# Optimization experiments

Hardware: AMD Instinct MI355X
Metric: run time of the kernel (lower is better)

Reference implementation:

```python
import jax, jax.numpy as jnp
import numpy as np

NEG_SLOPE = 0.1

def _leaky(x):
    return jnp.where(x >= 0, x, NEG_SLOPE * x)

def setup_inputs() -> dict:
    key = jax.random.key(0)
    ks = jax.random.split(key, 16)
    B, N, H, W, C = 4, 128, 32, 32, 64
    inp = {
        "image": jax.random.normal(ks[0], (B, 3, H, W), dtype=jnp.float32),
        "coords": jax.random.uniform(ks[1], (B, N, 2), dtype=jnp.float32),
        "w1": jax.random.normal(ks[2], (C, 7), dtype=jnp.float32) * 0.2,
        "b1": jax.random.normal(ks[3], (C,), dtype=jnp.float32) * 0.05,
        "w2": jax.random.normal(ks[4], (C, C), dtype=jnp.float32) * 0.1,
        "b2": jax.random.normal(ks[5], (C,), dtype=jnp.float32) * 0.05,
        "w3": jax.random.normal(ks[6], (C, C), dtype=jnp.float32) * 0.1,
        "b3": jax.random.normal(ks[7], (C,), dtype=jnp.float32) * 0.05,
        "w4": jax.random.normal(ks[8], (C, C), dtype=jnp.float32) * 0.1,
        "b4": jax.random.normal(ks[9], (C,), dtype=jnp.float32) * 0.05,
        "w5": jax.random.normal(ks[10], (C, C), dtype=jnp.float32) * 0.1,
        "b5": jax.random.normal(ks[11], (C,), dtype=jnp.float32) * 0.05,
        "wl": jax.random.normal(ks[12], (3, C), dtype=jnp.float32) * 0.1,
        "bl": jax.random.normal(ks[13], (3,), dtype=jnp.float32) * 0.05,
    }
    return inp

def reference(image, coords, w1, b1, w2, b2, w3, b3, w4, b4, w5, b5, wl, bl):
    B, C_img, H, W = image.shape
    _, N, D = coords.shape
    # position encoding: channel 0 = row/(H-1), channel 1 = col/(W-1)
    row = (jnp.arange(H, dtype=jnp.float32) / (H - 1))[:, None] * jnp.ones((1, W), jnp.float32)
    col = jnp.ones((H, 1), jnp.float32) * (jnp.arange(W, dtype=jnp.float32) / (W - 1))[None, :]
    pos = jnp.stack([row, col], axis=0)  # [2,H,W]
    # x5: [B,5,H,W] = image ++ pos
    x5 = jnp.concatenate([image, jnp.broadcast_to(pos[None], (B, 2, H, W))], axis=1)
    # First 1x1 conv: split weight into image/pos part (5 ch) and coord part (2 ch);
    # avoids materializing the expanded [B*N,7,H,W] input (same math as conv on concat).
    img_part = jnp.einsum('oc,bchw->bohw', w1[:, :5], x5)          # [B,c,H,W]
    crd_part = jnp.einsum('od,bnd->bno', w1[:, 5:], coords)         # [B,N,c]
    h = _leaky(img_part[:, None] + crd_part[:, :, :, None, None] + b1[None, None, :, None, None])  # [B,N,c,H,W]
    for wi, bi in ((w2, b2), (w3, b3), (w4, b4), (w5, b5)):
        h = _leaky(jnp.einsum('oc,bnchw->bnohw', wi, h) + bi[None, None, :, None, None])
    pooled = jnp.mean(h, axis=(-2, -1))                             # [B,N,c] (AdaptiveAvgPool2d(1,1)+Flatten)
    pred = jax.nn.sigmoid(jnp.einsum('oc,bnc->bno', wl, pooled) + bl)  # [B,N,3]
    return jnp.transpose(pred, (0, 2, 1))                           # [B,3,N]
```

## Files before the change

kernel.cpp:

```cpp
#include <hip/hip_runtime.h>
#include <math.h>


typedef float  f32x4  __attribute__((ext_vector_type(4)));
typedef f32x4  f32x4a __attribute__((may_alias));
typedef __bf16 bf16x8 __attribute__((ext_vector_type(8)));
typedef bf16x8 bf16x8a __attribute__((may_alias));
typedef __bf16 bf16x4 __attribute__((ext_vector_type(4)));
typedef bf16x4 bf16x4a __attribute__((may_alias));
typedef float  floata __attribute__((may_alias));

#define MFMA16(a, b, c) __builtin_amdgcn_mfma_f32_16x16x32_bf16((a), (b), (c), 0, 0, 0)

#define WL_H    0
#define ACT_H   18432

__global__ __launch_bounds__(256, 2) void mlp_mfma_kernel(
    const float* __restrict__ image,
    const float* __restrict__ coords,
    const float* __restrict__ w1, const float* __restrict__ b1,
    const float* __restrict__ w2, const float* __restrict__ b2,
    const float* __restrict__ w3, const float* __restrict__ b3,
    const float* __restrict__ w4, const float* __restrict__ b4,
    const float* __restrict__ w5, const float* __restrict__ b5,
    const float* __restrict__ wl, const float* __restrict__ bl,
    float* __restrict__ out)
{
    __shared__ __align__(16) __bf16 LDSH[18432 + 16384];
    __shared__ __align__(16) float  BL[320];

    const int tid  = threadIdx.x;
    const int wave = tid >> 6;
    const int lane = tid & 63;
    const int c15  = lane & 15;
    const int q    = lane >> 4;
    const int bn   = blockIdx.x;
    const int b    = bn >> 7;

    const float qm = (q == 0) ? 1.0f : 0.0f;

    const float* Ws[4] = {w2, w3, w4, w5};

    #pragma unroll 1
    for (int i = 0; i < 9; ++i) {
        const int id = wave + i * 4;
        __bf16* dst = &LDSH[WL_H + id * 512 + lane * 8];
        if (id < 32) {
            const int l  = id >> 3;
            const int mt = (id >> 1) & 3;
            const int ks = id & 1;
            const float* src = Ws[l] + (mt * 16 + c15) * 64 + ks * 32 + q * 8;
            f32x4 lo = *(const f32x4a*)src;
            f32x4 hi = *(const f32x4a*)(src + 4);
            bf16x8 f;
            f[0] = (__bf16)lo[0]; f[1] = (__bf16)lo[1];
            f[2] = (__bf16)lo[2]; f[3] = (__bf16)lo[3];
            f[4] = (__bf16)hi[0]; f[5] = (__bf16)hi[1];
            f[6] = (__bf16)hi[2]; f[7] = (__bf16)hi[3];
            *(bf16x8a*)dst = f;
        } else {
            const int mt = id - 32;
            bf16x8 f;
            #pragma unroll
            for (int j = 0; j < 7; ++j)
                f[j] = (__bf16)(qm * w1[(mt * 16 + c15) * 7 + j]);
            f[7] = (__bf16)0.0f;
            *(bf16x8a*)dst = f;
        }
    }
    if (tid < 64) {
        BL[tid]       = b1[tid];
        BL[64 + tid]  = b2[tid];
        BL[128 + tid] = b3[tid];
        BL[192 + tid] = b4[tid];
        BL[256 + tid] = b5[tid];
    }
    __syncthreads();

    const float cx = coords[2 * bn + 0];
    const float cy = coords[2 * bn + 1];
    const float* img = image + b * 3072;

    __bf16* Xw = &LDSH[ACT_H + wave * 4096];
    const int lane_woff = c15 * 8 + (q >> 1) * 128 + (q & 1) * 4;

    f32x4 pool[4];
    #pragma unroll
    for (int mt = 0; mt < 4; ++mt) pool[mt] = (f32x4){0.f, 0.f, 0.f, 0.f};

    auto store_tile = [&](f32x4 (&acc)[4][2], int g) {
        #pragma unroll
        for (int mt = 0; mt < 4; ++mt)
            #pragma unroll
            for (int ntl = 0; ntl < 2; ++ntl) {
                f32x4 a = acc[mt][ntl];
                bf16x4 p;
                #pragma unroll
                for (int r = 0; r < 4; ++r) {
                    float v = fmaxf(a[r], 0.1f * a[r]);
                    p[r] = (__bf16)v;
                }
                const int off = g * 2048 + (ntl * 2 + (mt >> 1)) * 512
                              + (mt & 1) * 256 + lane_woff;
                *(bf16x4a*)&Xw[off] = p;
            }
    };

    #pragma unroll 1
    for (int t = 0; t < 4; ++t) {
        {
            bf16x8 a1[4];
            #pragma unroll
            for (int mt = 0; mt < 4; ++mt)
                a1[mt] = *(const bf16x8a*)&LDSH[WL_H + (32 + mt) * 512 + lane * 8];
            f32x4 bv[4];
            #pragma unroll
            for (int mt = 0; mt < 4; ++mt)
                bv[mt] = *(const f32x4a*)&BL[mt * 16 + 4 * q];

            #pragma unroll
            for (int g = 0; g < 2; ++g) {
                bf16x8 bft[2];
                #pragma unroll
                for (int ntl = 0; ntl < 2; ++ntl) {
                    const int hw = wave * 256 + t * 64 + g * 32 + ntl * 16 + c15;
                    const float i0 = img[hw];
                    const float i1 = img[1024 + hw];
                    const float i2 = img[2048 + hw];
                    bf16x8 f;
                    f[0] = (__bf16)(qm * i0);
                    f[1] = (__bf16)(qm * i1);
                    f[2] = (__bf16)(qm * i2);
                    f[3] = (__bf16)(qm * (float)(hw >> 5) * (1.0f / 31.0f));
                    f[4] = (__bf16)(qm * (float)(hw & 31) * (1.0f / 31.0f));
                    f[5] = (__bf16)(qm * cx);
                    f[6] = (__bf16)(qm * cy);
                    f[7] = (__bf16)0.0f;
                    bft[ntl] = f;
                }
                f32x4 acc[4][2];
                #pragma unroll
                for (int mt = 0; mt < 4; ++mt) {
                    acc[mt][0] = bv[mt]; acc[mt][1] = bv[mt];
                }
                #pragma unroll
                for (int mt = 0; mt < 4; ++mt)
                    #pragma unroll
                    for (int ntl = 0; ntl < 2; ++ntl)
                        acc[mt][ntl] = MFMA16(a1[mt], bft[ntl], acc[mt][ntl]);
                store_tile(acc, g);
            }
        }

        #pragma unroll 1
        for (int l = 0; l < 4; ++l) {
            bf16x8 af[4][2];
            #pragma unroll
            for (int mt = 0; mt < 4; ++mt)
                #pragma unroll
                for (int ks = 0; ks < 2; ++ks)
                    af[mt][ks] = *(const bf16x8a*)
                        &LDSH[WL_H + (l * 8 + mt * 2 + ks) * 512 + lane * 8];
            f32x4 bv[4];
            #pragma unroll
            for (int mt = 0; mt < 4; ++mt)
                bv[mt] = *(const f32x4a*)&BL[(l + 1) * 64 + mt * 16 + 4 * q];

            #pragma unroll
            for (int g = 0; g < 2; ++g) {
                bf16x8 bf[2][2];
                #pragma unroll
                for (int ntl = 0; ntl < 2; ++ntl)
                    #pragma unroll
                    for (int ks = 0; ks < 2; ++ks)
                        bf[ntl][ks] = *(const bf16x8a*)
                            &Xw[g * 2048 + ((ntl * 2 + ks) * 64 + lane) * 8];
                f32x4 acc[4][2];
                #pragma unroll
                for (int mt = 0; mt < 4; ++mt) {
                    acc[mt][0] = bv[mt]; acc[mt][1] = bv[mt];
                }
                #pragma unroll
                for (int mt = 0; mt < 4; ++mt)
                    #pragma unroll
                    for (int ntl = 0; ntl < 2; ++ntl)
                        #pragma unroll
                        for (int ks = 0; ks < 2; ++ks)
                            acc[mt][ntl] = MFMA16(af[mt][ks], bf[ntl][ks], acc[mt][ntl]);
                if (l < 3) {
                    store_tile(acc, g);
                } else {
                    #pragma unroll
                    for (int mt = 0; mt < 4; ++mt)
                        #pragma unroll
                        for (int ntl = 0; ntl < 2; ++ntl) {
                            f32x4 a = acc[mt][ntl];
                            #pragma unroll
                            for (int r = 0; r < 4; ++r)
                                pool[mt][r] += fmaxf(a[r], 0.1f * a[r]);
                        }
                }
            }
        }
    }

    floata* Xf = (floata*)Xw;
    #pragma unroll
    for (int mt = 0; mt < 4; ++mt)
        #pragma unroll
        for (int r = 0; r < 4; ++r)
            Xf[(mt * 16 + 4 * q + r) * 16 + c15] = pool[mt][r];

    __syncthreads();

    if (tid < 64) {
        const int c = tid;
        float s = 0.0f;
        #pragma unroll
        for (int w = 0; w < 4; ++w) {
            const floata* P = (const floata*)&LDSH[ACT_H + w * 4096];
            #pragma unroll
            for (int c4 = 0; c4 < 4; ++c4) {
                f32x4 v = *(const f32x4a*)&P[c * 16 + c4 * 4];
                s += v[0] + v[1] + v[2] + v[3];
            }
        }
        const float p = s * (1.0f / 1024.0f);
        float s0 = wl[c] * p;
        float s1 = wl[64 + c] * p;
        float s2 = wl[128 + c] * p;
        #pragma unroll
        for (int off = 32; off > 0; off >>= 1) {
            s0 += __shfl_down(s0, off, 64);
            s1 += __shfl_down(s1, off, 64);
            s2 += __shfl_down(s2, off, 64);
        }
        if (c == 0) {
            const int n = bn & 127;
            out[(b * 3 + 0) * 128 + n] = 1.0f / (1.0f + expf(-(bl[0] + s0)));
            out[(b * 3 + 1) * 128 + n] = 1.0f / (1.0f + expf(-(bl[1] + s1)));
            out[(b * 3 + 2) * 128 + n] = 1.0f / (1.0f + expf(-(bl[2] + s2)));
        }
    }
}

extern "C" void kernel_launch(void* const* d_in, const int* in_sizes, int n_in,
                              void* d_out, int out_size, void* d_ws, size_t ws_size,
                              hipStream_t stream) {
    const float* image  = (const float*)d_in[0];
    const float* coords = (const float*)d_in[1];
    const float* w1 = (const float*)d_in[2];
    const float* b1 = (const float*)d_in[3];
    const float* w2 = (const float*)d_in[4];
    const float* b2 = (const float*)d_in[5];
    const float* w3 = (const float*)d_in[6];
    const float* b3 = (const float*)d_in[7];
    const float* w4 = (const float*)d_in[8];
    const float* b4 = (const float*)d_in[9];
    const float* w5 = (const float*)d_in[10];
    const float* b5 = (const float*)d_in[11];
    const float* wl = (const float*)d_in[12];
    const float* bl = (const float*)d_in[13];
    float* out = (float*)d_out;

    mlp_mfma_kernel<<<dim3(512), dim3(256), 0, stream>>>(
        image, coords, w1, b1, w2, b2, w3, b3, w4, b4, w5, b5, wl, bl, out);
}
```

Baseline: 110.5 us.

## Prestage bf16 weights in a separate kernel and double waves per block

Moves the fp32-to-bf16 weight fragment conversion out of every block into a one-block pre-kernel that writes the fragments to workspace. The main kernel now loads weight fragments from global memory (L2-cached) instead of LDS, and the LDS weight region is removed. Each block now runs 8 waves of 512 threads, each covering half as many pixels, which increases parallelism per block. The costs are an extra kernel launch, global-memory reads of weights inside the layer loop, and a higher register and occupancy demand from the 512-thread blocks.

Result: slower. 114.7 us (+3.8%).

```diff
diff --git a/kernel.cpp b/kernel.cpp
--- a/kernel.cpp
+++ b/kernel.cpp
@@ -12,39 +12,23 @@
 
 #define MFMA16(a, b, c) __builtin_amdgcn_mfma_f32_16x16x32_bf16((a), (b), (c), 0, 0, 0)
 
-#define WL_H    0
-#define ACT_H   18432
-
-__global__ __launch_bounds__(256, 2) void mlp_mfma_kernel(
-    const float* __restrict__ image,
-    const float* __restrict__ coords,
-    const float* __restrict__ w1, const float* __restrict__ b1,
-    const float* __restrict__ w2, const float* __restrict__ b2,
-    const float* __restrict__ w3, const float* __restrict__ b3,
-    const float* __restrict__ w4, const float* __restrict__ b4,
-    const float* __restrict__ w5, const float* __restrict__ b5,
-    const float* __restrict__ wl, const float* __restrict__ bl,
-    float* __restrict__ out)
+__global__ __launch_bounds__(256) void stage_weights_kernel(
+    const float* __restrict__ w1, const float* __restrict__ w2,
+    const float* __restrict__ w3, const float* __restrict__ w4,
+    const float* __restrict__ w5, __bf16* __restrict__ ws)
 {
-    __shared__ __align__(16) __bf16 LDSH[18432 + 16384];
-    __shared__ __align__(16) float  BL[320];
-
     const int tid  = threadIdx.x;
     const int wave = tid >> 6;
     const int lane = tid & 63;
     const int c15  = lane & 15;
     const int q    = lane >> 4;
-    const int bn   = blockIdx.x;
-    const int b    = bn >> 7;
-
     const float qm = (q == 0) ? 1.0f : 0.0f;
-
     const float* Ws[4] = {w2, w3, w4, w5};
 
     #pragma unroll 1
     for (int i = 0; i < 9; ++i) {
         const int id = wave + i * 4;
-        __bf16* dst = &LDSH[WL_H + id * 512 + lane * 8];
+        __bf16* dst = ws + id * 512 + lane * 8;
         if (id < 32) {
             const int l  = id >> 3;
             const int mt = (id >> 1) & 3;
@@ -68,6 +52,31 @@
             *(bf16x8a*)dst = f;
         }
     }
+}
+
+__global__ __launch_bounds__(512, 2) void mlp_mfma_kernel(
+    const float* __restrict__ image,
+    const float* __restrict__ coords,
+    const float* __restrict__ b1, const float* __restrict__ b2,
+    const float* __restrict__ b3, const float* __restrict__ b4,
+    const float* __restrict__ b5,
+    const float* __restrict__ wl, const float* __restrict__ bl,
+    const __bf16* __restrict__ ws,
+    float* __restrict__ out)
+{
+    __shared__ __align__(16) __bf16 LDSH[8 * 4096];
+    __shared__ __align__(16) float  BL[320];
+
+    const int tid  = threadIdx.x;
+    const int wave = tid >> 6;
+    const int lane = tid & 63;
+    const int c15  = lane & 15;
+    const int q    = lane >> 4;
+    const int bn   = blockIdx.x;
+    const int b    = bn >> 7;
+
+    const float qm = (q == 0) ? 1.0f : 0.0f;
+
     if (tid < 64) {
         BL[tid]       = b1[tid];
         BL[64 + tid]  = b2[tid];
@@ -77,11 +86,16 @@
     }
     __syncthreads();
 
+    bf16x8 a1[4];
+    #pragma unroll
+    for (int mt = 0; mt < 4; ++mt)
+        a1[mt] = *(const bf16x8a*)&ws[(32 + mt) * 512 + lane * 8];
+
     const float cx = coords[2 * bn + 0];
     const float cy = coords[2 * bn + 1];
     const float* img = image + b * 3072;
 
-    __bf16* Xw = &LDSH[ACT_H + wave * 4096];
+    __bf16* Xw = &LDSH[wave * 4096];
     const int lane_woff = c15 * 8 + (q >> 1) * 128 + (q & 1) * 4;
 
     f32x4 pool[4];
@@ -107,12 +121,8 @@
     };
 
     #pragma unroll 1
-    for (int t = 0; t < 4; ++t) {
+    for (int t = 0; t < 2; ++t) {
         {
-            bf16x8 a1[4];
-            #pragma unroll
-            for (int mt = 0; mt < 4; ++mt)
-                a1[mt] = *(const bf16x8a*)&LDSH[WL_H + (32 + mt) * 512 + lane * 8];
             f32x4 bv[4];
             #pragma unroll
             for (int mt = 0; mt < 4; ++mt)
@@ -123,7 +133,7 @@
                 bf16x8 bft[2];
                 #pragma unroll
                 for (int ntl = 0; ntl < 2; ++ntl) {
-                    const int hw = wave * 256 + t * 64 + g * 32 + ntl * 16 + c15;
+                    const int hw = wave * 128 + t * 64 + g * 32 + ntl * 16 + c15;
                     const float i0 = img[hw];
                     const float i1 = img[1024 + hw];
                     const float i2 = img[2048 + hw];
@@ -160,7 +170,7 @@
                 #pragma unroll
                 for (int ks = 0; ks < 2; ++ks)
                     af[mt][ks] = *(const bf16x8a*)
-                        &LDSH[WL_H + (l * 8 + mt * 2 + ks) * 512 + lane * 8];
+                        &ws[(l * 8 + mt * 2 + ks) * 512 + lane * 8];
             f32x4 bv[4];
             #pragma unroll
             for (int mt = 0; mt < 4; ++mt)
@@ -217,8 +227,8 @@
         const int c = tid;
         float s = 0.0f;
         #pragma unroll
-        for (int w = 0; w < 4; ++w) {
-            const floata* P = (const floata*)&LDSH[ACT_H + w * 4096];
+        for (int w = 0; w < 8; ++w) {
+            const floata* P = (const floata*)&LDSH[w * 4096];
             #pragma unroll
             for (int c4 = 0; c4 < 4; ++c4) {
                 f32x4 v = *(const f32x4a*)&P[c * 16 + c4 * 4];
@@ -262,7 +272,9 @@
     const float* wl = (const float*)d_in[12];
     const float* bl = (const float*)d_in[13];
     float* out = (float*)d_out;
-
-    mlp_mfma_kernel<<<dim3(512), dim3(256), 0, stream>>>(
-        image, coords, w1, b1, w2, b2, w3, b3, w4, b4, w5, b5, wl, bl, out);
+    __bf16* ws = (__bf16*)d_ws;
+
+    stage_weights_kernel<<<dim3(1), dim3(256), 0, stream>>>(w1, w2, w3, w4, w5, ws);
+    mlp_mfma_kernel<<<dim3(512), dim3(512), 0, stream>>>(
+        image, coords, b1, b2, b3, b4, b5, wl, bl, ws, out);
 }
```
